# Kernel optimization log

Measured on AMD Instinct MI355X. Metric: run time of the kernel, lower is better.

## Reference

```python
import jax, jax.numpy as jnp
import numpy as np

B, D, H, W = 16, 512, 32, 32   # batch, input_dim, spatial
CD, K = 256, 8192              # codebook dim, num codes
COMMIT = 1.0


def setup_inputs() -> dict:
    key = jax.random.key(0)
    k0, k1, k2, k3 = jax.random.split(key, 4)
    x = jax.random.normal(k0, (B, D, H, W), dtype=jnp.float32)
    # project_in: Linear(D -> CD); project_out: Linear(CD -> D)
    W_in = jax.random.normal(k1, (CD, D), dtype=jnp.float32) * (1.0 / np.sqrt(D))
    b_in = jnp.zeros((CD,), dtype=jnp.float32)
    W_out = jax.random.normal(k2, (D, CD), dtype=jnp.float32) * (1.0 / np.sqrt(CD))
    b_out = jnp.zeros((D,), dtype=jnp.float32)
    codebook = jax.random.normal(k3, (K, CD), dtype=jnp.float32) * 0.05
    return {"x": x, "W_in": W_in, "b_in": b_in, "W_out": W_out,
            "b_out": b_out, "codebook": codebook}


def reference(x, W_in, b_in, W_out, b_out, codebook):
    b, d, h, w = x.shape
    # b d h w -> b (h w) d
    xt = x.reshape(b, d, h * w).transpose(0, 2, 1)
    z = xt @ W_in.T + b_in                              # [b, n, CD]
    # squared euclidean distances to all codes: ||z||^2 - 2 z.e + ||e||^2
    d2 = ((z * z).sum(-1, keepdims=True)
          - 2.0 * jnp.einsum('bnc,kc->bnk', z, codebook)
          + (codebook * codebook).sum(-1))              # [b, n, K]
    indices = jnp.argmin(d2, axis=-1)                   # [b, n] int
    q = codebook[indices]                               # [b, n, CD]
    # training branch: commitment loss + straight-through estimator
    commitment_loss = COMMIT * jnp.mean((jax.lax.stop_gradient(q) - z) ** 2)
    q_ste = z + jax.lax.stop_gradient(q - z)
    out = q_ste @ W_out.T + b_out                       # [b, n, d]
    out = out.transpose(0, 2, 1).reshape(b, d, h, w)    # b (h w) d -> b d h w
    return out, indices, commitment_loss
```

## Files before the change

kernel.cpp:

```cpp
#include <hip/hip_runtime.h>
#include <cfloat>
#include <cstdint>

#define B_      16
#define DIN     512
#define HW      1024
#define CDIM    256
#define KCODES  8192
#define NTOK    (B_ * HW)
#define OUT_ELEMS (B_ * DIN * HW)
#define NSTRIP  8
#define NPART2  16
#define CPS     (KCODES / NSTRIP)
#define MAXR    4096
#define RCHUNK  32
#define RBLOCKS 2048
#define LOSS_SCALE (1.0f / ((float)NTOK * (float)CDIM))
#define WSCALE      16.0f
#define INV_WS      0.0625f
#define INV_WS2     0.00390625f
#define NEG2_INV_WS (-0.125f)
#define BAND_SLACK  2e-3f
#define A_BYTES  131072
#define B_OFF    131072
#define EE_OFF   (131072 + 3 * 8192)
#define LDS_TOT  (EE_OFF + 4096)
#define PO_BOFF  65536
#define PO_TOT   163840

typedef __attribute__((ext_vector_type(8))) _Float16 f16x8;
typedef __attribute__((ext_vector_type(4))) float f32x4;

static __device__ __forceinline__ short f2h(float f) {
  _Float16 h = (_Float16)f;
  return __builtin_bit_cast(short, h);
}
static __device__ __forceinline__ float h2f(short h) {
  return (float)__builtin_bit_cast(_Float16, h);
}

#define GLL16(gsrc, ldst)                                                      \
  __builtin_amdgcn_global_load_lds(                                           \
      (const __attribute__((address_space(1))) unsigned int*)(gsrc),          \
      (__attribute__((address_space(3))) unsigned int*)(ldst), 16, 0, 0)

#define PREP_CB_BLKS 2048
#define PREP_W_BLKS  128
#define PREP_X_BLKS  2048
__global__ __launch_bounds__(256) void k_prep(
    const float* __restrict__ cb, const float* __restrict__ Win,
    const float* __restrict__ Wout, const float* __restrict__ x,
    short* __restrict__ cb_hi, short* __restrict__ cb_lo, float* __restrict__ ee,
    short* __restrict__ wi_hi, short* __restrict__ wi_lo,
    short* __restrict__ wo_hi,
    short* __restrict__ xT_hi, short* __restrict__ xT_lo,
    float* __restrict__ loss, int* __restrict__ rcount, int* __restrict__ scal) {
  __shared__ float T[64][65];
  const int blk = blockIdx.x;
  const int tid = threadIdx.x;
  if (blk == 0 && tid < 2) {
    if (tid == 0) *loss = 0.0f; else *rcount = 0;
  }
  if (blk < PREP_CB_BLKS) {
    const int wid = (blk * 256 + tid) >> 6;
    const int lane = tid & 63;
    const float4 v = *(const float4*)(cb + (size_t)wid * CDIM + lane * 4);
    float s = v.x * v.x + v.y * v.y + v.z * v.z + v.w * v.w;
    const float sx = v.x * WSCALE, sy = v.y * WSCALE,
                sz = v.z * WSCALE, sw = v.w * WSCALE;
    short4 h, l;
    h.x = f2h(sx); l.x = f2h(sx - h2f(h.x));
    h.y = f2h(sy); l.y = f2h(sy - h2f(h.y));
    h.z = f2h(sz); l.z = f2h(sz - h2f(h.z));
    h.w = f2h(sw); l.w = f2h(sw - h2f(h.w));
    *(short4*)(cb_hi + (size_t)wid * CDIM + lane * 4) = h;
    *(short4*)(cb_lo + (size_t)wid * CDIM + lane * 4) = l;
    const float rx = v.x - h2f(h.x) * INV_WS;
    const float ry = v.y - h2f(h.y) * INV_WS;
    const float rz = v.z - h2f(h.z) * INV_WS;
    const float rw = v.w - h2f(h.w) * INV_WS;
    float rr = rx * rx + ry * ry + rz * rz + rw * rw;
#pragma unroll
    for (int off = 32; off > 0; off >>= 1) {
      s += __shfl_down(s, off, 64);
      rr += __shfl_down(rr, off, 64);
    }
    const int wv = tid >> 6;
    if (lane == 0) { ee[wid] = s; T[0][wv] = s; T[1][wv] = rr; }
    __syncthreads();
    if (tid == 0) {
      const float em = fmaxf(fmaxf(T[0][0], T[0][1]), fmaxf(T[0][2], T[0][3]));
      const float rm = fmaxf(fmaxf(T[1][0], T[1][1]), fmaxf(T[1][2], T[1][3]));
      atomicMax(scal + 0, __float_as_int(em));
      atomicMax(scal + 1, __float_as_int(rm));
    }
  } else if (blk < PREP_CB_BLKS + PREP_W_BLKS) {
    const int i = ((blk - PREP_CB_BLKS) * 256 + tid) * 4;
    {
      const float4 v = *(const float4*)(Win + i);
      const float sx = v.x * WSCALE, sy = v.y * WSCALE,
                  sz = v.z * WSCALE, sw = v.w * WSCALE;
      short4 h, l;
      h.x = f2h(sx); l.x = f2h(sx - h2f(h.x));
      h.y = f2h(sy); l.y = f2h(sy - h2f(h.y));
      h.z = f2h(sz); l.z = f2h(sz - h2f(h.z));
      h.w = f2h(sw); l.w = f2h(sw - h2f(h.w));
      *(short4*)(wi_hi + i) = h; *(short4*)(wi_lo + i) = l;
    }
    {
      const float4 v = *(const float4*)(Wout + i);
      short4 h;
      h.x = f2h(v.x * WSCALE);
      h.y = f2h(v.y * WSCALE);
      h.z = f2h(v.z * WSCALE);
      h.w = f2h(v.w * WSCALE);
      *(short4*)(wo_hi + i) = h;
    }
  } else {
    const int id = blk - PREP_CB_BLKS - PREP_W_BLKS;
    const int xb = id & 255, yb = id >> 8;
    const int b = xb >> 4;
    const int hw0 = (xb & 15) * 64;
    const int din0 = yb * 64;
    {
      const int r = tid >> 2;
      const int c = tid & 3;
      const float* src = x + ((size_t)b * DIN + din0 + r) * HW + hw0 + c * 16;
#pragma unroll
      for (int j = 0; j < 4; ++j) {
        const float4 v = *(const float4*)(src + j * 4);
        T[r][c * 16 + j * 4 + 0] = v.x;
        T[r][c * 16 + j * 4 + 1] = v.y;
        T[r][c * 16 + j * 4 + 2] = v.z;
        T[r][c * 16 + j * 4 + 3] = v.w;
      }
    }
    __syncthreads();
    {
      const int tt = tid & 63;
      const int c2 = tid >> 6;
      short h[16], l[16];
#pragma unroll
      for (int j = 0; j < 16; ++j) {
        const float f = T[c2 * 16 + j][tt];
        h[j] = f2h(f); l[j] = f2h(f - h2f(h[j]));
      }
      const size_t base = ((size_t)b * HW + hw0 + tt) * DIN + din0 + c2 * 16;
      *(f16x8*)(xT_hi + base)     = *(f16x8*)&h[0];
      *(f16x8*)(xT_hi + base + 8) = *(f16x8*)&h[8];
      *(f16x8*)(xT_lo + base)     = *(f16x8*)&l[0];
      *(f16x8*)(xT_lo + base + 8) = *(f16x8*)&l[8];
    }
  }
}

__global__ __launch_bounds__(256, 2) void k_proj_in_mfma(
    const short* __restrict__ xT_hi, const short* __restrict__ xT_lo,
    const short* __restrict__ wi_hi, const short* __restrict__ wi_lo,
    const float* __restrict__ bin,
    short* __restrict__ z_hi, short* __restrict__ z_lo) {
  __shared__ short lds_s[4 * 128 * 32];
  char* ldsc = (char*)lds_s;
  const int tid = threadIdx.x;
  const int w = tid >> 6, lane = tid & 63;
  const int quad = lane >> 4, l16 = lane & 15;
  const int wm = w >> 1, wn = w & 1;
  const int tok0 = blockIdx.x * 128;
  const int cd0 = blockIdx.y * 128;

  const int uA = (w << 6) + lane, uB = uA + 256;
  const int tA = uA >> 2, pA = uA & 3, qA = pA ^ ((tA >> 1) & 3);
  const int tB = uB >> 2, pB = uB & 3, qB = pB ^ ((tB >> 1) & 3);
  const int offA = tA * DIN + qA * 8;
  const int offB = tB * DIN + qB * 8;
  const short* gAh0 = xT_hi + (size_t)tok0 * DIN + offA;
  const short* gAh1 = xT_hi + (size_t)tok0 * DIN + offB;
  const short* gAl0 = xT_lo + (size_t)tok0 * DIN + offA;
  const short* gAl1 = xT_lo + (size_t)tok0 * DIN + offB;
  const short* gBh0 = wi_hi + (size_t)cd0 * DIN + offA;
  const short* gBh1 = wi_hi + (size_t)cd0 * DIN + offB;
  const short* gBl0 = wi_lo + (size_t)cd0 * DIN + offA;
  const short* gBl1 = wi_lo + (size_t)cd0 * DIN + offB;

  int aoffs[4], boffs[4];
#pragma unroll
  for (int mi = 0; mi < 4; ++mi) {
    const int t = wm * 64 + mi * 16 + l16;
    aoffs[mi] = t * 64 + (quad ^ ((t >> 1) & 3)) * 16;
  }
#pragma unroll
  for (int ni = 0; ni < 4; ++ni) {
    const int t = wn * 64 + ni * 16 + l16;
    boffs[ni] = 16384 + t * 64 + (quad ^ ((t >> 1) & 3)) * 16;
  }

  f32x4 acc[4][4];
#pragma unroll
  for (int mi = 0; mi < 4; ++mi)
#pragma unroll
    for (int ni = 0; ni < 4; ++ni) acc[mi][ni] = (f32x4){0.f, 0.f, 0.f, 0.f};

  for (int kb = 0; kb < DIN; kb += 32) {
    __syncthreads();
    GLL16(gAh0 + kb, ldsc + ((0 * 4 + w) << 10));
    GLL16(gAh1 + kb, ldsc + ((1 * 4 + w) << 10));
    GLL16(gAl0 + kb, ldsc + ((2 * 4 + w) << 10));
    GLL16(gAl1 + kb, ldsc + ((3 * 4 + w) << 10));
    GLL16(gBh0 + kb, ldsc + ((4 * 4 + w) << 10));
    GLL16(gBh1 + kb, ldsc + ((5 * 4 + w) << 10));
    GLL16(gBl0 + kb, ldsc + ((6 * 4 + w) << 10));
    GLL16(gBl1 + kb, ldsc + ((7 * 4 + w) << 10));
    __syncthreads();
    f16x8 ah[4], al[4], bh[4], bl[4];
#pragma unroll
    for (int mi = 0; mi < 4; ++mi) {
      ah[mi] = *(const f16x8*)(ldsc + aoffs[mi]);
      al[mi] = *(const f16x8*)(ldsc + 8192 + aoffs[mi]);
    }
#pragma unroll
    for (int ni = 0; ni < 4; ++ni) {
      bh[ni] = *(const f16x8*)(ldsc + boffs[ni]);
      bl[ni] = *(const f16x8*)(ldsc + 8192 + boffs[ni]);
    }
#pragma unroll
    for (int mi = 0; mi < 4; ++mi)
#pragma unroll
      for (int ni = 0; ni < 4; ++ni) {
        f32x4 c = acc[mi][ni];
        c = __builtin_amdgcn_mfma_f32_16x16x32_f16(ah[mi], bh[ni], c, 0, 0, 0);
        c = __builtin_amdgcn_mfma_f32_16x16x32_f16(ah[mi], bl[ni], c, 0, 0, 0);
        c = __builtin_amdgcn_mfma_f32_16x16x32_f16(al[mi], bh[ni], c, 0, 0, 0);
        acc[mi][ni] = c;
      }
  }
  float bv[4];
#pragma unroll
  for (int ni = 0; ni < 4; ++ni) bv[ni] = bin[cd0 + wn * 64 + ni * 16 + l16];
#pragma unroll
  for (int mi = 0; mi < 4; ++mi)
#pragma unroll
    for (int r = 0; r < 4; ++r) {
      const int t = tok0 + wm * 64 + mi * 16 + quad * 4 + r;
#pragma unroll
      for (int ni = 0; ni < 4; ++ni) {
        const int cd = cd0 + wn * 64 + ni * 16 + l16;
        const float o = acc[mi][ni][r] * INV_WS + bv[ni];
        const short h = f2h(o);
        z_hi[(size_t)t * CDIM + cd] = h;
        z_lo[(size_t)t * CDIM + cd] = f2h(o - h2f(h));
      }
    }
}

__global__ __launch_bounds__(512, 2) void k_argmin_mfma(
    const short* __restrict__ z_hi,
    const short* __restrict__ cb_hi,
    const float* __restrict__ ee,
    float* __restrict__ pm1v, int* __restrict__ pm1i, float* __restrict__ pm2v) {
  __shared__ short lds_s[LDS_TOT / 2];
  char* ldsc = (char*)lds_s;
  const int tid = threadIdx.x;
  const int w = tid >> 6, lane = tid & 63;
  const int quad = lane >> 4, l16 = lane & 15;
  const int wm = w >> 1, wn = w & 1;
  const int tok0 = blockIdx.x * 256;
  const int cbase = blockIdx.y * CPS;

#pragma unroll
  for (int r = 0; r < 16; ++r) {
    const int u = r * 512 + tid;
    const int c = u >> 10, t = (u >> 2) & 255, p = u & 3;
    const int q = p ^ ((t >> 1) & 3);
    GLL16(z_hi + (size_t)(tok0 + t) * CDIM + c * 32 + q * 8,
          ldsc + r * 8192 + (w << 10));
  }
  if (w < 4) {
    GLL16(ee + cbase + w * 256 + lane * 4, ldsc + EE_OFF + (w << 10));
  }
  const int crB = tid >> 2, pB = tid & 3;
  const int qB = pB ^ ((crB >> 1) & 3);
  const short* bsrc = cb_hi + (size_t)(cbase + crB) * CDIM + qB * 8;
  GLL16(bsrc, ldsc + B_OFF + (w << 10));
  GLL16(bsrc + 32, ldsc + B_OFF + 8192 + (w << 10));

  int aoffs[4], boffs[4];
#pragma unroll
  for (int mi = 0; mi < 4; ++mi) {
    const int t = wm * 64 + mi * 16 + l16;
    aoffs[mi] = t * 64 + (quad ^ ((t >> 1) & 3)) * 16;
  }
#pragma unroll
  for (int ni = 0; ni < 4; ++ni) {
    const int t = wn * 64 + ni * 16 + l16;
    boffs[ni] = t * 64 + (quad ^ ((t >> 1) & 3)) * 16;
  }
  const float* eelds = (const float*)(ldsc + EE_OFF);

  float mv[16], sv[16]; int mi_[16];
#pragma unroll
  for (int j = 0; j < 16; ++j) {
    mv[j] = FLT_MAX; sv[j] = FLT_MAX; mi_[j] = 0x7fffffff;
  }

  int cur = 0;
  for (int ct = 0; ct < 8; ++ct) {
    f32x4 acc[4][4];
#pragma unroll
    for (int mi = 0; mi < 4; ++mi)
#pragma unroll
      for (int ni = 0; ni < 4; ++ni) acc[mi][ni] = (f32x4){0.f, 0.f, 0.f, 0.f};

#pragma unroll
    for (int kbi = 0; kbi < 8; ++kbi) {
      const int s = ct * 8 + kbi;
      asm volatile("s_waitcnt vmcnt(1)" ::: "memory");
      __builtin_amdgcn_s_barrier();
      __builtin_amdgcn_sched_barrier(0);
      {
        const int s2 = (s + 2) & 63;
        const int nslot = cur + 2 - ((cur >= 1) ? 3 : 0);
        GLL16(bsrc + (size_t)(s2 >> 3) * 128 * CDIM + (s2 & 7) * 32,
              ldsc + B_OFF + (nslot << 13) + (w << 10));
      }
      const int abase = kbi << 14;
      const int bbase = B_OFF + (cur << 13);
      f16x8 ah[4], bh[4];
#pragma unroll
      for (int mi = 0; mi < 4; ++mi)
        ah[mi] = *(const f16x8*)(ldsc + abase + aoffs[mi]);
#pragma unroll
      for (int ni = 0; ni < 4; ++ni)
        bh[ni] = *(const f16x8*)(ldsc + bbase + boffs[ni]);
#pragma unroll
      for (int mi = 0; mi < 4; ++mi)
#pragma unroll
        for (int ni = 0; ni < 4; ++ni)
          acc[mi][ni] = __builtin_amdgcn_mfma_f32_16x16x32_f16(
              ah[mi], bh[ni], acc[mi][ni], 0, 0, 0);
      cur = (cur == 2) ? 0 : cur + 1;
    }
    const int ctile = cbase + ct * 128;
    float eev[4];
#pragma unroll
    for (int ni = 0; ni < 4; ++ni)
      eev[ni] = eelds[ct * 128 + wn * 64 + ni * 16 + l16];
    const int cb2 = ctile + wn * 64 + l16;
#pragma unroll
    for (int mi = 0; mi < 4; ++mi)
#pragma unroll
      for (int r = 0; r < 4; ++r) {
        const int j = mi * 4 + r;
#pragma unroll
        for (int ni = 0; ni < 4; ++ni) {
          const float s = fmaf(NEG2_INV_WS, acc[mi][ni][r], eev[ni]);
          sv[j] = fminf(sv[j], fmaxf(mv[j], s));
          if (s < mv[j]) { mv[j] = s; mi_[j] = cb2 + ni * 16; }
        }
      }
  }
#pragma unroll
  for (int off = 1; off < 16; off <<= 1) {
#pragma unroll
    for (int j = 0; j < 16; ++j) {
      const float ov = __shfl_xor(mv[j], off, 64);
      const int   oi = __shfl_xor(mi_[j], off, 64);
      const float os = __shfl_xor(sv[j], off, 64);
      const float snew = fminf(fminf(sv[j], os), fmaxf(mv[j], ov));
      if (ov < mv[j] || (ov == mv[j] && oi < mi_[j])) { mv[j] = ov; mi_[j] = oi; }
      sv[j] = snew;
    }
  }
  if (l16 == 0) {
    const int p = blockIdx.y * 2 + wn;
#pragma unroll
    for (int j = 0; j < 16; ++j) {
      const int mi = j >> 2, r = j & 3;
      const int t = tok0 + wm * 64 + mi * 16 + quad * 4 + r;
      const size_t o = (size_t)p * NTOK + t;
      pm1v[o] = mv[j]; pm1i[o] = mi_[j]; pm2v[o] = sv[j];
    }
  }
}

__global__ __launch_bounds__(256) void k_merge_rescue(
    const float* __restrict__ pm1v, const int* __restrict__ pm1i,
    const float* __restrict__ pm2v,
    const short* __restrict__ z_hi, const short* __restrict__ z_lo,
    const float* __restrict__ cb, const int* __restrict__ scal,
    int* __restrict__ idxi, float* __restrict__ idx_f,
    int* __restrict__ rlist, int* __restrict__ rcount,
    float* __restrict__ loss) {
  __shared__ float lpart[4];
  const int tid = threadIdx.x;
  const int wv = tid >> 6, lane = tid & 63;
  const int t = blockIdx.x * 4 + wv;
  float av = FLT_MAX, asv = FLT_MAX; int ai = 0x7fffffff;
  if (lane < NPART2) {
    const size_t po = (size_t)lane * NTOK + t;
    av = pm1v[po]; ai = pm1i[po]; asv = pm2v[po];
  }
  float m1v = av; int m1i = ai; float msv = asv;
#pragma unroll
  for (int off = 1; off < 64; off <<= 1) {
    const float ov = __shfl_xor(m1v, off, 64);
    const int   oi = __shfl_xor(m1i, off, 64);
    const float os = __shfl_xor(msv, off, 64);
    msv = fminf(msv, os);
    if (ov < m1v || (ov == m1v && oi < m1i)) { m1v = ov; m1i = oi; }
  }
  const short4 h4 = *(const short4*)(z_hi + (size_t)t * CDIM + lane * 4);
  const short4 l4 = *(const short4*)(z_lo + (size_t)t * CDIM + lane * 4);
  const float hx = h2f(h4.x), hy = h2f(h4.y), hz = h2f(h4.z), hw = h2f(h4.w);
  const float lx = h2f(l4.x), ly = h2f(l4.y), lz = h2f(l4.z), lw = h2f(l4.w);
  const float zx = hx + lx, zy = hy + ly, zz = hz + lz, zw = hw + lw;
  float zl2 = lx * lx + ly * ly + lz * lz + lw * lw;
  float zh2 = hx * hx + hy * hy + hz * hz + hw * hw;
#pragma unroll
  for (int off = 32; off > 0; off >>= 1) {
    zl2 += __shfl_xor(zl2, off, 64);
    zh2 += __shfl_xor(zh2, off, 64);
  }
  const float emax = sqrtf(__int_as_float(scal[0]));
  const float rmax = sqrtf(__int_as_float(scal[1]));
  const float band = 4.0f * (sqrtf(zl2) * emax + sqrtf(zh2) * rmax) + BAND_SLACK;
  const float thr = m1v + band;
  const unsigned long long ball = __ballot(av <= thr);
  const bool flag = (msv <= thr);
  int besti = m1i;
  if (__popcll(ball) > 1) {
    double bestv = 1e300; int bi = 0x7fffffff;
    unsigned long long bb = ball;
    while (bb) {
      const int c = __ffsll((long long)bb) - 1;
      bb &= bb - 1;
      const int ci = __shfl(ai, c, 64);
      const float4 ev = *(const float4*)(cb + (size_t)ci * CDIM + lane * 4);
      const double dx = (double)zx - (double)ev.x;
      const double dy = (double)zy - (double)ev.y;
      const double dz_ = (double)zz - (double)ev.z;
      const double dw = (double)zw - (double)ev.w;
      double d = dx * dx + dy * dy + dz_ * dz_ + dw * dw;
#pragma unroll
      for (int off = 32; off > 0; off >>= 1) d += __shfl_xor(d, off, 64);
      if (d < bestv || (d == bestv && ci < bi)) { bestv = d; bi = ci; }
    }
    besti = bi;
  }
  const float4 qv = *(const float4*)(cb + (size_t)besti * CDIM + lane * 4);
  const float dx = qv.x - zx;
  const float dy = qv.y - zy;
  const float dz_ = qv.z - zz;
  const float dw = qv.w - zw;
  float s = dx * dx + dy * dy + dz_ * dz_ + dw * dw;
#pragma unroll
  for (int off = 32; off > 0; off >>= 1) s += __shfl_down(s, off, 64);
  if (lane == 0) {
    idxi[t] = besti;
    idx_f[t] = (float)besti;
    lpart[wv] = s;
    if (flag) {
      const int pos = atomicAdd(rcount, 1);
      if (pos < MAXR) rlist[pos] = t;
    }
  }
  __syncthreads();
  if (tid == 0) {
    atomicAdd(loss, (lpart[0] + lpart[1] + lpart[2] + lpart[3]) * LOSS_SCALE);
  }
}

__global__ __launch_bounds__(256) void k_rescue_chunk(
    const short* __restrict__ z_hi, const short* __restrict__ z_lo,
    const float* __restrict__ cb,
    const int* __restrict__ rlist, const int* __restrict__ rcount,
    double* __restrict__ slotv, int* __restrict__ sloti) {
  const int cnt0 = *rcount;
  const int cnt = cnt0 < MAXR ? cnt0 : MAXR;
  const int li0 = blockIdx.x >> 5;
  const int chunk = blockIdx.x & (RCHUNK - 1);
  if (li0 >= cnt) return;
  __shared__ float zrow[CDIM];
  __shared__ double rv[256];
  __shared__ int ri[256];
  const int tid = threadIdx.x;
  for (int li = li0; li < cnt; li += RBLOCKS / RCHUNK) {
    const int t = rlist[li];
    zrow[tid] = h2f(z_hi[(size_t)t * CDIM + tid]) + h2f(z_lo[(size_t)t * CDIM + tid]);
    __syncthreads();
    const int k = chunk * 256 + tid;
    const float* e = cb + (size_t)k * CDIM;
    double s0 = 0.0, s1 = 0.0, s2 = 0.0, s3 = 0.0;
    for (int c = 0; c < CDIM; c += 4) {
      const float4 ev = *(const float4*)(e + c);
      const double d0 = (double)zrow[c]     - (double)ev.x;
      const double d1 = (double)zrow[c + 1] - (double)ev.y;
      const double d2 = (double)zrow[c + 2] - (double)ev.z;
      const double d3 = (double)zrow[c + 3] - (double)ev.w;
      s0 += d0 * d0; s1 += d1 * d1; s2 += d2 * d2; s3 += d3 * d3;
    }
    rv[tid] = (s0 + s1) + (s2 + s3);
    ri[tid] = k;
    __syncthreads();
    for (int off = 128; off > 0; off >>= 1) {
      if (tid < off) {
        if (rv[tid + off] < rv[tid] ||
            (rv[tid + off] == rv[tid] && ri[tid + off] < ri[tid])) {
          rv[tid] = rv[tid + off]; ri[tid] = ri[tid + off];
        }
      }
      __syncthreads();
    }
    if (tid == 0) {
      slotv[(size_t)li * RCHUNK + chunk] = rv[0];
      sloti[(size_t)li * RCHUNK + chunk] = ri[0];
    }
    __syncthreads();
  }
}

__global__ __launch_bounds__(256) void k_rescue_fin(
    const double* __restrict__ slotv, const int* __restrict__ sloti,
    const int* __restrict__ rlist, const int* __restrict__ rcount,
    const short* __restrict__ z_hi, const short* __restrict__ z_lo,
    const float* __restrict__ cb,
    int* __restrict__ idxi, float* __restrict__ idx_f, float* __restrict__ loss) {
  const int cnt0 = *rcount;
  const int cnt = cnt0 < MAXR ? cnt0 : MAXR;
  const int tid = threadIdx.x;
  const int wv = tid >> 6, lane = tid & 63;
  for (int li = wv; li < cnt; li += 4) {
    double bv = 1e300; int bx = 0x7fffffff;
    if (lane < RCHUNK) {
      bv = slotv[(size_t)li * RCHUNK + lane];
      bx = sloti[(size_t)li * RCHUNK + lane];
    }
#pragma unroll
    for (int off = 1; off < 32; off <<= 1) {
      const double ov = __shfl_xor(bv, off, 64);
      const int   oi = __shfl_xor(bx, off, 64);
      if (ov < bv || (ov == bv && oi < bx)) { bv = ov; bx = oi; }
    }
    const int newi = __shfl(bx, 0, 64);
    const int t = rlist[li];
    const int oldi = idxi[t];
    if (newi != oldi) {
      const short4 h4 = *(const short4*)(z_hi + (size_t)t * CDIM + lane * 4);
      const short4 l4 = *(const short4*)(z_lo + (size_t)t * CDIM + lane * 4);
      const float4 qn = *(const float4*)(cb + (size_t)newi * CDIM + lane * 4);
      const float4 qo = *(const float4*)(cb + (size_t)oldi * CDIM + lane * 4);
      const float zx = h2f(h4.x) + h2f(l4.x);
      const float zy = h2f(h4.y) + h2f(l4.y);
      const float zz = h2f(h4.z) + h2f(l4.z);
      const float zw = h2f(h4.w) + h2f(l4.w);
      float d = (qn.x - zx) * (qn.x - zx) - (qo.x - zx) * (qo.x - zx)
              + (qn.y - zy) * (qn.y - zy) - (qo.y - zy) * (qo.y - zy)
              + (qn.z - zz) * (qn.z - zz) - (qo.z - zz) * (qo.z - zz)
              + (qn.w - zw) * (qn.w - zw) - (qo.w - zw) * (qo.w - zw);
#pragma unroll
      for (int off = 32; off > 0; off >>= 1) d += __shfl_down(d, off, 64);
      if (lane == 0) {
        idxi[t] = newi;
        idx_f[t] = (float)newi;
        atomicAdd(loss, d * LOSS_SCALE);
      }
    }
  }
}

__global__ __launch_bounds__(512, 2) void k_proj_out_mfma(
    const short* __restrict__ wo_hi,
    const short* __restrict__ cb_hi, const short* __restrict__ cb_lo,
    const int* __restrict__ idxi, const float* __restrict__ bout,
    float* __restrict__ out) {
  __shared__ short lds_s[PO_TOT / 2];
  char* ldsc = (char*)lds_s;
  const int tid = threadIdx.x;
  const int w = tid >> 6, lane = tid & 63;
  const int quad = lane >> 4, l16 = lane & 15;
  const int wm = w >> 2, wn = w & 3;
  const int tok0 = blockIdx.x * 256;
  const int din0 = blockIdx.y * 128;

  const int tr = tid >> 2, p = tid & 3;
  const int q = p ^ ((tr >> 1) & 3);
  const int i0 = idxi[tok0 + tr];
  const int i1 = idxi[tok0 + 128 + tr];
  const short* s0h = cb_hi + (size_t)i0 * CDIM + q * 8;
  const short* s1h = cb_hi + (size_t)i1 * CDIM + q * 8;
  const short* s0l = cb_lo + (size_t)i0 * CDIM + q * 8;
  const short* s1l = cb_lo + (size_t)i1 * CDIM + q * 8;

#pragma unroll
  for (int c = 0; c < 8; ++c)
    GLL16(wo_hi + (size_t)(din0 + tr) * CDIM + c * 32 + q * 8,
          ldsc + c * 8192 + (w << 10));

#define PO_STAGE(s_, slot_)                                                    \
  {                                                                            \
    char* bb_ = ldsc + PO_BOFF + ((slot_) << 15);                              \
    GLL16(s0h + (s_) * 32, bb_ + (w << 10));                                   \
    GLL16(s1h + (s_) * 32, bb_ + 8192 + (w << 10));                            \
    GLL16(s0l + (s_) * 32, bb_ + 16384 + (w << 10));                           \
    GLL16(s1l + (s_) * 32, bb_ + 24576 + (w << 10));                           \
  }
  PO_STAGE(0, 0);
  PO_STAGE(1, 1);

  int aoffs[4], boffs[4];
#pragma unroll
  for (int mi = 0; mi < 4; ++mi) {
    const int t = wm * 64 + mi * 16 + l16;
    aoffs[mi] = t * 64 + (quad ^ ((t >> 1) & 3)) * 16;
  }
#pragma unroll
  for (int ni = 0; ni < 4; ++ni) {
    const int t = wn * 64 + ni * 16 + l16;
    boffs[ni] = t * 64 + (quad ^ ((t >> 1) & 3)) * 16;
  }

  f32x4 acc[4][4];
#pragma unroll
  for (int mi = 0; mi < 4; ++mi)
#pragma unroll
    for (int ni = 0; ni < 4; ++ni) acc[mi][ni] = (f32x4){0.f, 0.f, 0.f, 0.f};

  int cur = 0;
#pragma unroll
  for (int s = 0; s < 8; ++s) {
    asm volatile("s_waitcnt vmcnt(4)" ::: "memory");
    __builtin_amdgcn_s_barrier();
    __builtin_amdgcn_sched_barrier(0);
    {
      const int s2 = (s + 2) & 7;
      const int nslot = cur + 2 - ((cur >= 1) ? 3 : 0);
      PO_STAGE(s2, nslot);
    }
    const int abase = s << 13;
    const int bbase = PO_BOFF + (cur << 15);
    f16x8 ah[4], bh[4], bl[4];
#pragma unroll
    for (int mi = 0; mi < 4; ++mi)
      ah[mi] = *(const f16x8*)(ldsc + abase + aoffs[mi]);
#pragma unroll
    for (int ni = 0; ni < 4; ++ni) {
      bh[ni] = *(const f16x8*)(ldsc + bbase + boffs[ni]);
      bl[ni] = *(const f16x8*)(ldsc + bbase + 16384 + boffs[ni]);
    }
#pragma unroll
    for (int mi = 0; mi < 4; ++mi)
#pragma unroll
      for (int ni = 0; ni < 4; ++ni) {
        f32x4 c = acc[mi][ni];
        c = __builtin_amdgcn_mfma_f32_16x16x32_f16(ah[mi], bh[ni], c, 0, 0, 0);
        c = __builtin_amdgcn_mfma_f32_16x16x32_f16(ah[mi], bl[ni], c, 0, 0, 0);
        acc[mi][ni] = c;
      }
    cur = (cur == 2) ? 0 : cur + 1;
  }
#undef PO_STAGE

  const int b = tok0 >> 10;
  const int hwb = tok0 & (HW - 1);
  float* ob = out + (size_t)b * DIN * HW;
#pragma unroll
  for (int mi = 0; mi < 4; ++mi)
#pragma unroll
    for (int r = 0; r < 4; ++r) {
      const int din = din0 + wm * 64 + mi * 16 + quad * 4 + r;
      const float bb = bout[din];
#pragma unroll
      for (int ni = 0; ni < 4; ++ni) {
        const int hw = hwb + wn * 64 + ni * 16 + l16;
        ob[(size_t)din * HW + hw] = acc[mi][ni][r] * INV_WS2 + bb;
      }
    }
}

extern "C" void kernel_launch(void* const* d_in, const int* in_sizes, int n_in,
                              void* d_out, int out_size, void* d_ws, size_t ws_size,
                              hipStream_t stream) {
  const float* x    = (const float*)d_in[0];
  const float* Win  = (const float*)d_in[1];
  const float* bin  = (const float*)d_in[2];
  const float* Wout = (const float*)d_in[3];
  const float* bout = (const float*)d_in[4];
  const float* cb   = (const float*)d_in[5];

  float* out   = (float*)d_out;
  float* idx_f = out + OUT_ELEMS;
  float* loss  = out + OUT_ELEMS + NTOK;

  char* w = (char*)d_ws;
  size_t off = 0;
  short* z_hi  = (short*)(w + off); off += (size_t)NTOK * CDIM * 2;
  short* z_lo  = (short*)(w + off); off += (size_t)NTOK * CDIM * 2;
  short* cb_hi = (short*)(w + off); off += (size_t)KCODES * CDIM * 2;
  short* cb_lo = (short*)(w + off); off += (size_t)KCODES * CDIM * 2;
  short* xT_hi = (short*)(w + off); off += (size_t)NTOK * DIN * 2;
  short* xT_lo = (short*)(w + off); off += (size_t)NTOK * DIN * 2;
  short* wi_hi = (short*)(w + off); off += (size_t)CDIM * DIN * 2;
  short* wi_lo = (short*)(w + off); off += (size_t)CDIM * DIN * 2;
  short* wo_hi = (short*)(w + off); off += (size_t)DIN * CDIM * 2;
  float* ee    = (float*)(w + off); off += (size_t)KCODES * 4;
  int*   idxi  = (int*)(w + off);   off += (size_t)NTOK * 4;
  float* pm1v  = (float*)(w + off); off += (size_t)NPART2 * NTOK * 4;
  int*   pm1i  = (int*)(w + off);   off += (size_t)NPART2 * NTOK * 4;
  float* pm2v  = (float*)(w + off); off += (size_t)NPART2 * NTOK * 4;
  int*   rlist = (int*)(w + off);   off += (size_t)MAXR * 4;
  int*   rcount= (int*)(w + off);   off += 256;
  int*   scal  = (int*)(w + off);   off += 256;
  double* slotv= (double*)(w + off);off += (size_t)MAXR * RCHUNK * 8;
  int*   sloti = (int*)(w + off);   off += (size_t)MAXR * RCHUNK * 4;

  hipMemsetAsync(scal, 0, 8, stream);
  k_prep        <<<dim3(PREP_CB_BLKS + PREP_W_BLKS + PREP_X_BLKS),
                   dim3(256), 0, stream>>>(cb, Win, Wout, x, cb_hi, cb_lo, ee,
                                           wi_hi, wi_lo, wo_hi,
                                           xT_hi, xT_lo, loss, rcount, scal);
  k_proj_in_mfma<<<dim3(NTOK / 128, CDIM / 128), dim3(256), 0, stream>>>(
      xT_hi, xT_lo, wi_hi, wi_lo, bin, z_hi, z_lo);
  k_argmin_mfma <<<dim3(NTOK / 256, NSTRIP), dim3(512), 0, stream>>>(
      z_hi, cb_hi, ee, pm1v, pm1i, pm2v);
  k_merge_rescue<<<dim3(NTOK / 4), dim3(256), 0, stream>>>(
      pm1v, pm1i, pm2v, z_hi, z_lo, cb, scal, idxi, idx_f,
      rlist, rcount, loss);
  k_rescue_chunk<<<dim3(RBLOCKS), dim3(256), 0, stream>>>(
      z_hi, z_lo, cb, rlist, rcount, slotv, sloti);
  k_rescue_fin  <<<dim3(1), dim3(256), 0, stream>>>(
      slotv, sloti, rlist, rcount, z_hi, z_lo, cb, idxi, idx_f, loss);
  k_proj_out_mfma<<<dim3(NTOK / 256, DIN / 128), dim3(512), 0, stream>>>(
      wo_hi, cb_hi, cb_lo, idxi, bout, out);
}
```

Measured before the change: 431.3 us.

## Reorder rescue after proj_out, fuse rescue kernels, patch outputs with delta correction

```diff
diff --git a/kernel.cpp b/kernel.cpp
--- a/kernel.cpp
+++ b/kernel.cpp
@@ -54,12 +54,15 @@
     short* __restrict__ wi_hi, short* __restrict__ wi_lo,
     short* __restrict__ wo_hi,
     short* __restrict__ xT_hi, short* __restrict__ xT_lo,
-    float* __restrict__ loss, int* __restrict__ rcount, int* __restrict__ scal) {
+    float* __restrict__ loss, int* __restrict__ rcount, int* __restrict__ done,
+    float* __restrict__ scalE, float* __restrict__ scalR) {
   __shared__ float T[64][65];
   const int blk = blockIdx.x;
   const int tid = threadIdx.x;
-  if (blk == 0 && tid < 2) {
-    if (tid == 0) *loss = 0.0f; else *rcount = 0;
+  if (blk == 0 && tid < 3) {
+    if (tid == 0) *loss = 0.0f;
+    else if (tid == 1) *rcount = 0;
+    else *done = 0;
   }
   if (blk < PREP_CB_BLKS) {
     const int wid = (blk * 256 + tid) >> 6;
@@ -89,10 +92,8 @@
     if (lane == 0) { ee[wid] = s; T[0][wv] = s; T[1][wv] = rr; }
     __syncthreads();
     if (tid == 0) {
-      const float em = fmaxf(fmaxf(T[0][0], T[0][1]), fmaxf(T[0][2], T[0][3]));
-      const float rm = fmaxf(fmaxf(T[1][0], T[1][1]), fmaxf(T[1][2], T[1][3]));
-      atomicMax(scal + 0, __float_as_int(em));
-      atomicMax(scal + 1, __float_as_int(rm));
+      scalE[blk] = fmaxf(fmaxf(T[0][0], T[0][1]), fmaxf(T[0][2], T[0][3]));
+      scalR[blk] = fmaxf(fmaxf(T[1][0], T[1][1]), fmaxf(T[1][2], T[1][3]));
     }
   } else if (blk < PREP_CB_BLKS + PREP_W_BLKS) {
     const int i = ((blk - PREP_CB_BLKS) * 256 + tid) * 4;
@@ -158,10 +159,32 @@
     const short* __restrict__ xT_hi, const short* __restrict__ xT_lo,
     const short* __restrict__ wi_hi, const short* __restrict__ wi_lo,
     const float* __restrict__ bin,
-    short* __restrict__ z_hi, short* __restrict__ z_lo) {
+    short* __restrict__ z_hi, short* __restrict__ z_lo,
+    const float* __restrict__ scalE, const float* __restrict__ scalR,
+    float* __restrict__ scalG) {
   __shared__ short lds_s[4 * 128 * 32];
   char* ldsc = (char*)lds_s;
   const int tid = threadIdx.x;
+  if (blockIdx.x == 0 && blockIdx.y == 0) {
+    float em = 0.f, rm = 0.f;
+#pragma unroll
+    for (int i = 0; i < 8; ++i) {
+      em = fmaxf(em, scalE[tid * 8 + i]);
+      rm = fmaxf(rm, scalR[tid * 8 + i]);
+    }
+#pragma unroll
+    for (int off = 32; off > 0; off >>= 1) {
+      em = fmaxf(em, __shfl_xor(em, off, 64));
+      rm = fmaxf(rm, __shfl_xor(rm, off, 64));
+    }
+    float* sred = (float*)ldsc;
+    if ((tid & 63) == 0) { sred[tid >> 6] = em; sred[4 + (tid >> 6)] = rm; }
+    __syncthreads();
+    if (tid == 0) {
+      scalG[0] = fmaxf(fmaxf(sred[0], sred[1]), fmaxf(sred[2], sred[3]));
+      scalG[1] = fmaxf(fmaxf(sred[4], sred[5]), fmaxf(sred[6], sred[7]));
+    }
+  }
   const int w = tid >> 6, lane = tid & 63;
   const int quad = lane >> 4, l16 = lane & 15;
   const int wm = w >> 1, wn = w & 1;
@@ -376,7 +399,7 @@
     for (int j = 0; j < 16; ++j) {
       const int mi = j >> 2, r = j & 3;
       const int t = tok0 + wm * 64 + mi * 16 + quad * 4 + r;
-      const size_t o = (size_t)p * NTOK + t;
+      const size_t o = (size_t)t * NPART2 + p;
       pm1v[o] = mv[j]; pm1i[o] = mi_[j]; pm2v[o] = sv[j];
     }
   }
@@ -386,7 +409,7 @@
     const float* __restrict__ pm1v, const int* __restrict__ pm1i,
     const float* __restrict__ pm2v,
     const short* __restrict__ z_hi, const short* __restrict__ z_lo,
-    const float* __restrict__ cb, const int* __restrict__ scal,
+    const float* __restrict__ cb, const float* __restrict__ scalG,
     int* __restrict__ idxi, float* __restrict__ idx_f,
     int* __restrict__ rlist, int* __restrict__ rcount,
     float* __restrict__ loss) {
@@ -396,7 +419,7 @@
   const int t = blockIdx.x * 4 + wv;
   float av = FLT_MAX, asv = FLT_MAX; int ai = 0x7fffffff;
   if (lane < NPART2) {
-    const size_t po = (size_t)lane * NTOK + t;
+    const size_t po = (size_t)t * NPART2 + lane;
     av = pm1v[po]; ai = pm1i[po]; asv = pm2v[po];
   }
   float m1v = av; int m1i = ai; float msv = asv;
@@ -420,8 +443,8 @@
     zl2 += __shfl_xor(zl2, off, 64);
     zh2 += __shfl_xor(zh2, off, 64);
   }
-  const float emax = sqrtf(__int_as_float(scal[0]));
-  const float rmax = sqrtf(__int_as_float(scal[1]));
+  const float emax = sqrtf(scalG[0]);
+  const float rmax = sqrtf(scalG[1]);
   const float band = 4.0f * (sqrtf(zl2) * emax + sqrtf(zh2) * rmax) + BAND_SLACK;
   const float thr = m1v + band;
   const unsigned long long ball = __ballot(av <= thr);
@@ -469,64 +492,173 @@
   }
 }
 
-__global__ __launch_bounds__(256) void k_rescue_chunk(
+__global__ __launch_bounds__(512, 2) void k_proj_out_mfma(
+    const short* __restrict__ wo_hi,
+    const short* __restrict__ cb_hi, const short* __restrict__ cb_lo,
+    const int* __restrict__ idxi, const float* __restrict__ bout,
+    float* __restrict__ out) {
+  __shared__ short lds_s[PO_TOT / 2];
+  char* ldsc = (char*)lds_s;
+  const int tid = threadIdx.x;
+  const int w = tid >> 6, lane = tid & 63;
+  const int quad = lane >> 4, l16 = lane & 15;
+  const int wm = w >> 2, wn = w & 3;
+  const int tok0 = blockIdx.x * 256;
+  const int din0 = blockIdx.y * 128;
+
+  const int tr = tid >> 2, p = tid & 3;
+  const int q = p ^ ((tr >> 1) & 3);
+  const int i0 = idxi[tok0 + tr];
+  const int i1 = idxi[tok0 + 128 + tr];
+  const short* s0h = cb_hi + (size_t)i0 * CDIM + q * 8;
+  const short* s1h = cb_hi + (size_t)i1 * CDIM + q * 8;
+  const short* s0l = cb_lo + (size_t)i0 * CDIM + q * 8;
+  const short* s1l = cb_lo + (size_t)i1 * CDIM + q * 8;
+
+#pragma unroll
+  for (int c = 0; c < 8; ++c)
+    GLL16(wo_hi + (size_t)(din0 + tr) * CDIM + c * 32 + q * 8,
+          ldsc + c * 8192 + (w << 10));
+
+#define PO_STAGE(s_, slot_)                                                    \
+  {                                                                            \
+    char* bb_ = ldsc + PO_BOFF + ((slot_) << 15);                              \
+    GLL16(s0h + (s_) * 32, bb_ + (w << 10));                                   \
+    GLL16(s1h + (s_) * 32, bb_ + 8192 + (w << 10));                            \
+    GLL16(s0l + (s_) * 32, bb_ + 16384 + (w << 10));                           \
+    GLL16(s1l + (s_) * 32, bb_ + 24576 + (w << 10));                           \
+  }
+  PO_STAGE(0, 0);
+  PO_STAGE(1, 1);
+
+  int aoffs[4], boffs[4];
+#pragma unroll
+  for (int mi = 0; mi < 4; ++mi) {
+    const int t = wm * 64 + mi * 16 + l16;
+    aoffs[mi] = t * 64 + (quad ^ ((t >> 1) & 3)) * 16;
+  }
+#pragma unroll
+  for (int ni = 0; ni < 4; ++ni) {
+    const int t = wn * 64 + ni * 16 + l16;
+    boffs[ni] = t * 64 + (quad ^ ((t >> 1) & 3)) * 16;
+  }
+
+  f32x4 acc[4][4];
+#pragma unroll
+  for (int mi = 0; mi < 4; ++mi)
+#pragma unroll
+    for (int ni = 0; ni < 4; ++ni) acc[mi][ni] = (f32x4){0.f, 0.f, 0.f, 0.f};
+
+  int cur = 0;
+#pragma unroll
+  for (int s = 0; s < 8; ++s) {
+    asm volatile("s_waitcnt vmcnt(4)" ::: "memory");
+    __builtin_amdgcn_s_barrier();
+    __builtin_amdgcn_sched_barrier(0);
+    {
+      const int s2 = (s + 2) & 7;
+      const int nslot = cur + 2 - ((cur >= 1) ? 3 : 0);
+      PO_STAGE(s2, nslot);
+    }
+    const int abase = s << 13;
+    const int bbase = PO_BOFF + (cur << 15);
+    f16x8 ah[4], bh[4], bl[4];
+#pragma unroll
+    for (int mi = 0; mi < 4; ++mi)
+      ah[mi] = *(const f16x8*)(ldsc + abase + aoffs[mi]);
+#pragma unroll
+    for (int ni = 0; ni < 4; ++ni) {
+      bh[ni] = *(const f16x8*)(ldsc + bbase + boffs[ni]);
+      bl[ni] = *(const f16x8*)(ldsc + bbase + 16384 + boffs[ni]);
+    }
+#pragma unroll
+    for (int mi = 0; mi < 4; ++mi)
+#pragma unroll
+      for (int ni = 0; ni < 4; ++ni) {
+        f32x4 c = acc[mi][ni];
+        c = __builtin_amdgcn_mfma_f32_16x16x32_f16(ah[mi], bh[ni], c, 0, 0, 0);
+        c = __builtin_amdgcn_mfma_f32_16x16x32_f16(ah[mi], bl[ni], c, 0, 0, 0);
+        acc[mi][ni] = c;
+      }
+    cur = (cur == 2) ? 0 : cur + 1;
+  }
+#undef PO_STAGE
+
+  const int b = tok0 >> 10;
+  const int hwb = tok0 & (HW - 1);
+  float* ob = out + (size_t)b * DIN * HW;
+#pragma unroll
+  for (int mi = 0; mi < 4; ++mi)
+#pragma unroll
+    for (int r = 0; r < 4; ++r) {
+      const int din = din0 + wm * 64 + mi * 16 + quad * 4 + r;
+      const float bb = bout[din];
+#pragma unroll
+      for (int ni = 0; ni < 4; ++ni) {
+        const int hw = hwb + wn * 64 + ni * 16 + l16;
+        ob[(size_t)din * HW + hw] = acc[mi][ni][r] * INV_WS2 + bb;
+      }
+    }
+}
+
+__global__ __launch_bounds__(256) void k_rescue_chunk_fin(
     const short* __restrict__ z_hi, const short* __restrict__ z_lo,
     const float* __restrict__ cb,
     const int* __restrict__ rlist, const int* __restrict__ rcount,
-    double* __restrict__ slotv, int* __restrict__ sloti) {
+    double* __restrict__ slotv, int* __restrict__ sloti,
+    int* __restrict__ done,
+    int* __restrict__ idxi, float* __restrict__ idx_f, float* __restrict__ loss,
+    const float* __restrict__ Wout, float* __restrict__ out,
+    int* __restrict__ pold, int* __restrict__ pnew) {
   const int cnt0 = *rcount;
   const int cnt = cnt0 < MAXR ? cnt0 : MAXR;
   const int li0 = blockIdx.x >> 5;
   const int chunk = blockIdx.x & (RCHUNK - 1);
-  if (li0 >= cnt) return;
   __shared__ float zrow[CDIM];
   __shared__ double rv[256];
   __shared__ int ri[256];
+  __shared__ int isLast;
   const int tid = threadIdx.x;
-  for (int li = li0; li < cnt; li += RBLOCKS / RCHUNK) {
-    const int t = rlist[li];
-    zrow[tid] = h2f(z_hi[(size_t)t * CDIM + tid]) + h2f(z_lo[(size_t)t * CDIM + tid]);
-    __syncthreads();
-    const int k = chunk * 256 + tid;
-    const float* e = cb + (size_t)k * CDIM;
-    double s0 = 0.0, s1 = 0.0, s2 = 0.0, s3 = 0.0;
-    for (int c = 0; c < CDIM; c += 4) {
-      const float4 ev = *(const float4*)(e + c);
-      const double d0 = (double)zrow[c]     - (double)ev.x;
-      const double d1 = (double)zrow[c + 1] - (double)ev.y;
-      const double d2 = (double)zrow[c + 2] - (double)ev.z;
-      const double d3 = (double)zrow[c + 3] - (double)ev.w;
-      s0 += d0 * d0; s1 += d1 * d1; s2 += d2 * d2; s3 += d3 * d3;
-    }
-    rv[tid] = (s0 + s1) + (s2 + s3);
-    ri[tid] = k;
-    __syncthreads();
-    for (int off = 128; off > 0; off >>= 1) {
-      if (tid < off) {
-        if (rv[tid + off] < rv[tid] ||
-            (rv[tid + off] == rv[tid] && ri[tid + off] < ri[tid])) {
-          rv[tid] = rv[tid + off]; ri[tid] = ri[tid + off];
+  if (li0 < cnt) {
+    for (int li = li0; li < cnt; li += RBLOCKS / RCHUNK) {
+      const int t = rlist[li];
+      zrow[tid] = h2f(z_hi[(size_t)t * CDIM + tid]) + h2f(z_lo[(size_t)t * CDIM + tid]);
+      __syncthreads();
+      const int k = chunk * 256 + tid;
+      const float* e = cb + (size_t)k * CDIM;
+      double s0 = 0.0, s1 = 0.0, s2 = 0.0, s3 = 0.0;
+      for (int c = 0; c < CDIM; c += 4) {
+        const float4 ev = *(const float4*)(e + c);
+        const double d0 = (double)zrow[c]     - (double)ev.x;
+        const double d1 = (double)zrow[c + 1] - (double)ev.y;
+        const double d2 = (double)zrow[c + 2] - (double)ev.z;
+        const double d3 = (double)zrow[c + 3] - (double)ev.w;
+        s0 += d0 * d0; s1 += d1 * d1; s2 += d2 * d2; s3 += d3 * d3;
+      }
+      rv[tid] = (s0 + s1) + (s2 + s3);
+      ri[tid] = k;
+      __syncthreads();
+      for (int off = 128; off > 0; off >>= 1) {
+        if (tid < off) {
+          if (rv[tid + off] < rv[tid] ||
+              (rv[tid + off] == rv[tid] && ri[tid + off] < ri[tid])) {
+            rv[tid] = rv[tid + off]; ri[tid] = ri[tid + off];
+          }
         }
+        __syncthreads();
+      }
+      if (tid == 0) {
+        slotv[(size_t)li * RCHUNK + chunk] = rv[0];
+        sloti[(size_t)li * RCHUNK + chunk] = ri[0];
       }
       __syncthreads();
     }
-    if (tid == 0) {
-      slotv[(size_t)li * RCHUNK + chunk] = rv[0];
-      sloti[(size_t)li * RCHUNK + chunk] = ri[0];
-    }
-    __syncthreads();
-  }
-}
-
-__global__ __launch_bounds__(256) void k_rescue_fin(
-    const double* __restrict__ slotv, const int* __restrict__ sloti,
-    const int* __restrict__ rlist, const int* __restrict__ rcount,
-    const short* __restrict__ z_hi, const short* __restrict__ z_lo,
-    const float* __restrict__ cb,
-    int* __restrict__ idxi, float* __restrict__ idx_f, float* __restrict__ loss) {
-  const int cnt0 = *rcount;
-  const int cnt = cnt0 < MAXR ? cnt0 : MAXR;
-  const int tid = threadIdx.x;
+  }
+  __threadfence();
+  if (tid == 0) isLast = (atomicAdd(done, 1) == RBLOCKS - 1);
+  __syncthreads();
+  if (isLast == 0) return;
+  __threadfence();
   const int wv = tid >> 6, lane = tid & 63;
   for (int li = wv; li < cnt; li += 4) {
     double bv = 1e300; int bx = 0x7fffffff;
@@ -543,6 +675,7 @@
     const int newi = __shfl(bx, 0, 64);
     const int t = rlist[li];
     const int oldi = idxi[t];
+    if (lane == 0) { pold[li] = oldi; pnew[li] = newi; }
     if (newi != oldi) {
       const short4 h4 = *(const short4*)(z_hi + (size_t)t * CDIM + lane * 4);
       const short4 l4 = *(const short4*)(z_lo + (size_t)t * CDIM + lane * 4);
@@ -565,115 +698,30 @@
       }
     }
   }
-}
-
-__global__ __launch_bounds__(512, 2) void k_proj_out_mfma(
-    const short* __restrict__ wo_hi,
-    const short* __restrict__ cb_hi, const short* __restrict__ cb_lo,
-    const int* __restrict__ idxi, const float* __restrict__ bout,
-    float* __restrict__ out) {
-  __shared__ short lds_s[PO_TOT / 2];
-  char* ldsc = (char*)lds_s;
-  const int tid = threadIdx.x;
-  const int w = tid >> 6, lane = tid & 63;
-  const int quad = lane >> 4, l16 = lane & 15;
-  const int wm = w >> 2, wn = w & 3;
-  const int tok0 = blockIdx.x * 256;
-  const int din0 = blockIdx.y * 128;
-
-  const int tr = tid >> 2, p = tid & 3;
-  const int q = p ^ ((tr >> 1) & 3);
-  const int i0 = idxi[tok0 + tr];
-  const int i1 = idxi[tok0 + 128 + tr];
-  const short* s0h = cb_hi + (size_t)i0 * CDIM + q * 8;
-  const short* s1h = cb_hi + (size_t)i1 * CDIM + q * 8;
-  const short* s0l = cb_lo + (size_t)i0 * CDIM + q * 8;
-  const short* s1l = cb_lo + (size_t)i1 * CDIM + q * 8;
-
-#pragma unroll
-  for (int c = 0; c < 8; ++c)
-    GLL16(wo_hi + (size_t)(din0 + tr) * CDIM + c * 32 + q * 8,
-          ldsc + c * 8192 + (w << 10));
-
-#define PO_STAGE(s_, slot_)                                                    \
-  {                                                                            \
-    char* bb_ = ldsc + PO_BOFF + ((slot_) << 15);                              \
-    GLL16(s0h + (s_) * 32, bb_ + (w << 10));                                   \
-    GLL16(s1h + (s_) * 32, bb_ + 8192 + (w << 10));                            \
-    GLL16(s0l + (s_) * 32, bb_ + 16384 + (w << 10));                           \
-    GLL16(s1l + (s_) * 32, bb_ + 24576 + (w << 10));                           \
-  }
-  PO_STAGE(0, 0);
-  PO_STAGE(1, 1);
-
-  int aoffs[4], boffs[4];
-#pragma unroll
-  for (int mi = 0; mi < 4; ++mi) {
-    const int t = wm * 64 + mi * 16 + l16;
-    aoffs[mi] = t * 64 + (quad ^ ((t >> 1) & 3)) * 16;
-  }
-#pragma unroll
-  for (int ni = 0; ni < 4; ++ni) {
-    const int t = wn * 64 + ni * 16 + l16;
-    boffs[ni] = t * 64 + (quad ^ ((t >> 1) & 3)) * 16;
-  }
-
-  f32x4 acc[4][4];
-#pragma unroll
-  for (int mi = 0; mi < 4; ++mi)
-#pragma unroll
-    for (int ni = 0; ni < 4; ++ni) acc[mi][ni] = (f32x4){0.f, 0.f, 0.f, 0.f};
-
-  int cur = 0;
-#pragma unroll
-  for (int s = 0; s < 8; ++s) {
-    asm volatile("s_waitcnt vmcnt(4)" ::: "memory");
-    __builtin_amdgcn_s_barrier();
-    __builtin_amdgcn_sched_barrier(0);
-    {
-      const int s2 = (s + 2) & 7;
-      const int nslot = cur + 2 - ((cur >= 1) ? 3 : 0);
-      PO_STAGE(s2, nslot);
-    }
-    const int abase = s << 13;
-    const int bbase = PO_BOFF + (cur << 15);
-    f16x8 ah[4], bh[4], bl[4];
-#pragma unroll
-    for (int mi = 0; mi < 4; ++mi)
-      ah[mi] = *(const f16x8*)(ldsc + abase + aoffs[mi]);
-#pragma unroll
-    for (int ni = 0; ni < 4; ++ni) {
-      bh[ni] = *(const f16x8*)(ldsc + bbase + boffs[ni]);
-      bl[ni] = *(const f16x8*)(ldsc + bbase + 16384 + boffs[ni]);
-    }
-#pragma unroll
-    for (int mi = 0; mi < 4; ++mi)
-#pragma unroll
-      for (int ni = 0; ni < 4; ++ni) {
-        f32x4 c = acc[mi][ni];
-        c = __builtin_amdgcn_mfma_f32_16x16x32_f16(ah[mi], bh[ni], c, 0, 0, 0);
-        c = __builtin_amdgcn_mfma_f32_16x16x32_f16(ah[mi], bl[ni], c, 0, 0, 0);
-        acc[mi][ni] = c;
-      }
-    cur = (cur == 2) ? 0 : cur + 1;
-  }
-#undef PO_STAGE
-
-  const int b = tok0 >> 10;
-  const int hwb = tok0 & (HW - 1);
-  float* ob = out + (size_t)b * DIN * HW;
-#pragma unroll
-  for (int mi = 0; mi < 4; ++mi)
-#pragma unroll
-    for (int r = 0; r < 4; ++r) {
-      const int din = din0 + wm * 64 + mi * 16 + quad * 4 + r;
-      const float bb = bout[din];
-#pragma unroll
-      for (int ni = 0; ni < 4; ++ni) {
-        const int hw = hwb + wn * 64 + ni * 16 + l16;
-        ob[(size_t)din * HW + hw] = acc[mi][ni][r] * INV_WS2 + bb;
-      }
-    }
+  __syncthreads();
+  for (int li = 0; li < cnt; ++li) {
+    const int oldi = pold[li], newi = pnew[li];
+    if (oldi == newi) continue;
+    const int t = rlist[li];
+    const int b = t >> 10, hw = t & (HW - 1);
+    float* oc = out + (size_t)b * DIN * HW + hw;
+    const float* en = cb + (size_t)newi * CDIM;
+    const float* eo = cb + (size_t)oldi * CDIM;
+#pragma unroll
+    for (int rr2 = 0; rr2 < 2; ++rr2) {
+      const int din = tid + rr2 * 256;
+      const float* wr = Wout + (size_t)din * CDIM;
+      float d = 0.f;
+      for (int cdi = 0; cdi < CDIM; cdi += 4) {
+        const float4 wv4 = *(const float4*)(wr + cdi);
+        const float4 nv = *(const float4*)(en + cdi);
+        const float4 ov = *(const float4*)(eo + cdi);
+        d += wv4.x * (nv.x - ov.x) + wv4.y * (nv.y - ov.y)
+           + wv4.z * (nv.z - ov.z) + wv4.w * (nv.w - ov.w);
+      }
+      oc[(size_t)din * HW] += d;
+    }
+  }
 }
 
 extern "C" void kernel_launch(void* const* d_in, const int* in_sizes, int n_in,
@@ -708,26 +756,30 @@
   float* pm2v  = (float*)(w + off); off += (size_t)NPART2 * NTOK * 4;
   int*   rlist = (int*)(w + off);   off += (size_t)MAXR * 4;
   int*   rcount= (int*)(w + off);   off += 256;
-  int*   scal  = (int*)(w + off);   off += 256;
+  int*   done  = (int*)(w + off);   off += 256;
+  float* scalG = (float*)(w + off); off += 256;
+  float* scalE = (float*)(w + off); off += (size_t)PREP_CB_BLKS * 4;
+  float* scalR = (float*)(w + off); off += (size_t)PREP_CB_BLKS * 4;
+  int*   pold  = (int*)(w + off);   off += (size_t)MAXR * 4;
+  int*   pnew  = (int*)(w + off);   off += (size_t)MAXR * 4;
   double* slotv= (double*)(w + off);off += (size_t)MAXR * RCHUNK * 8;
   int*   sloti = (int*)(w + off);   off += (size_t)MAXR * RCHUNK * 4;
 
-  hipMemsetAsync(scal, 0, 8, stream);
   k_prep        <<<dim3(PREP_CB_BLKS + PREP_W_BLKS + PREP_X_BLKS),
                    dim3(256), 0, stream>>>(cb, Win, Wout, x, cb_hi, cb_lo, ee,
                                            wi_hi, wi_lo, wo_hi,
-                                           xT_hi, xT_lo, loss, rcount, scal);
+                                           xT_hi, xT_lo, loss, rcount, done,
+                                           scalE, scalR);
   k_proj_in_mfma<<<dim3(NTOK / 128, CDIM / 128), dim3(256), 0, stream>>>(
-      xT_hi, xT_lo, wi_hi, wi_lo, bin, z_hi, z_lo);
+      xT_hi, xT_lo, wi_hi, wi_lo, bin, z_hi, z_lo, scalE, scalR, scalG);
   k_argmin_mfma <<<dim3(NTOK / 256, NSTRIP), dim3(512), 0, stream>>>(
       z_hi, cb_hi, ee, pm1v, pm1i, pm2v);
   k_merge_rescue<<<dim3(NTOK / 4), dim3(256), 0, stream>>>(
-      pm1v, pm1i, pm2v, z_hi, z_lo, cb, scal, idxi, idx_f,
+      pm1v, pm1i, pm2v, z_hi, z_lo, cb, scalG, idxi, idx_f,
       rlist, rcount, loss);
-  k_rescue_chunk<<<dim3(RBLOCKS), dim3(256), 0, stream>>>(
-      z_hi, z_lo, cb, rlist, rcount, slotv, sloti);
-  k_rescue_fin  <<<dim3(1), dim3(256), 0, stream>>>(
-      slotv, sloti, rlist, rcount, z_hi, z_lo, cb, idxi, idx_f, loss);
   k_proj_out_mfma<<<dim3(NTOK / 256, DIN / 128), dim3(512), 0, stream>>>(
       wo_hi, cb_hi, cb_lo, idxi, bout, out);
-}
+  k_rescue_chunk_fin<<<dim3(RBLOCKS), dim3(256), 0, stream>>>(
+      z_hi, z_lo, cb, rlist, rcount, slotv, sloti, done,
+      idxi, idx_f, loss, Wout, out, pold, pnew);
+}
```

Measured after the change: 541.1 us. 1.25x slower.

## Triple-buffer proj_in LDS loads and raise wave priority around MFMA blocks

Applied to the files above, without the earlier changes.

```diff
diff --git a/kernel.cpp b/kernel.cpp
--- a/kernel.cpp
+++ b/kernel.cpp
@@ -159,7 +159,7 @@
     const short* __restrict__ wi_hi, const short* __restrict__ wi_lo,
     const float* __restrict__ bin,
     short* __restrict__ z_hi, short* __restrict__ z_lo) {
-  __shared__ short lds_s[4 * 128 * 32];
+  __shared__ short lds_s[3 * 16384];
   char* ldsc = (char*)lds_s;
   const int tid = threadIdx.x;
   const int w = tid >> 6, lane = tid & 63;
@@ -168,19 +168,32 @@
   const int tok0 = blockIdx.x * 128;
   const int cd0 = blockIdx.y * 128;
 
-  const int uA = (w << 6) + lane, uB = uA + 256;
-  const int tA = uA >> 2, pA = uA & 3, qA = pA ^ ((tA >> 1) & 3);
-  const int tB = uB >> 2, pB = uB & 3, qB = pB ^ ((tB >> 1) & 3);
-  const int offA = tA * DIN + qA * 8;
-  const int offB = tB * DIN + qB * 8;
-  const short* gAh0 = xT_hi + (size_t)tok0 * DIN + offA;
-  const short* gAh1 = xT_hi + (size_t)tok0 * DIN + offB;
-  const short* gAl0 = xT_lo + (size_t)tok0 * DIN + offA;
-  const short* gAl1 = xT_lo + (size_t)tok0 * DIN + offB;
-  const short* gBh0 = wi_hi + (size_t)cd0 * DIN + offA;
-  const short* gBh1 = wi_hi + (size_t)cd0 * DIN + offB;
-  const short* gBl0 = wi_lo + (size_t)cd0 * DIN + offA;
-  const short* gBl1 = wi_lo + (size_t)cd0 * DIN + offB;
+  const int t0 = tid >> 2, p0 = tid & 3, q0 = p0 ^ ((t0 >> 1) & 3);
+  const int u1 = tid + 256, t1 = u1 >> 2, p1 = u1 & 3, q1 = p1 ^ ((t1 >> 1) & 3);
+  const short* A0h = xT_hi + (size_t)(tok0 + t0) * DIN + q0 * 8;
+  const short* A1h = xT_hi + (size_t)(tok0 + t1) * DIN + q1 * 8;
+  const short* A0l = xT_lo + (size_t)(tok0 + t0) * DIN + q0 * 8;
+  const short* A1l = xT_lo + (size_t)(tok0 + t1) * DIN + q1 * 8;
+  const short* B0h = wi_hi + (size_t)(cd0 + t0) * DIN + q0 * 8;
+  const short* B1h = wi_hi + (size_t)(cd0 + t1) * DIN + q1 * 8;
+  const short* B0l = wi_lo + (size_t)(cd0 + t0) * DIN + q0 * 8;
+  const short* B1l = wi_lo + (size_t)(cd0 + t1) * DIN + q1 * 8;
+
+#define PI_STAGE(s_, slot_)                                                    \
+  {                                                                            \
+    char* bb_ = ldsc + ((slot_) << 15);                                        \
+    const int kb_ = (s_) * 32;                                                 \
+    GLL16(A0h + kb_, bb_ + (w << 10));                                         \
+    GLL16(A1h + kb_, bb_ + 4096 + (w << 10));                                  \
+    GLL16(A0l + kb_, bb_ + 8192 + (w << 10));                                  \
+    GLL16(A1l + kb_, bb_ + 12288 + (w << 10));                                 \
+    GLL16(B0h + kb_, bb_ + 16384 + (w << 10));                                 \
+    GLL16(B1h + kb_, bb_ + 20480 + (w << 10));                                 \
+    GLL16(B0l + kb_, bb_ + 24576 + (w << 10));                                 \
+    GLL16(B1l + kb_, bb_ + 28672 + (w << 10));                                 \
+  }
+  PI_STAGE(0, 0);
+  PI_STAGE(1, 1);
 
   int aoffs[4], boffs[4];
 #pragma unroll
@@ -200,28 +213,30 @@
 #pragma unroll
     for (int ni = 0; ni < 4; ++ni) acc[mi][ni] = (f32x4){0.f, 0.f, 0.f, 0.f};
 
-  for (int kb = 0; kb < DIN; kb += 32) {
-    __syncthreads();
-    GLL16(gAh0 + kb, ldsc + ((0 * 4 + w) << 10));
-    GLL16(gAh1 + kb, ldsc + ((1 * 4 + w) << 10));
-    GLL16(gAl0 + kb, ldsc + ((2 * 4 + w) << 10));
-    GLL16(gAl1 + kb, ldsc + ((3 * 4 + w) << 10));
-    GLL16(gBh0 + kb, ldsc + ((4 * 4 + w) << 10));
-    GLL16(gBh1 + kb, ldsc + ((5 * 4 + w) << 10));
-    GLL16(gBl0 + kb, ldsc + ((6 * 4 + w) << 10));
-    GLL16(gBl1 + kb, ldsc + ((7 * 4 + w) << 10));
-    __syncthreads();
+  int cur = 0;
+#pragma unroll
+  for (int s = 0; s < 16; ++s) {
+    asm volatile("s_waitcnt vmcnt(8)" ::: "memory");
+    __builtin_amdgcn_s_barrier();
+    __builtin_amdgcn_sched_barrier(0);
+    {
+      const int s2 = (s + 2) & 15;
+      const int nslot = cur + 2 - ((cur >= 1) ? 3 : 0);
+      PI_STAGE(s2, nslot);
+    }
+    const int bb = cur << 15;
     f16x8 ah[4], al[4], bh[4], bl[4];
 #pragma unroll
     for (int mi = 0; mi < 4; ++mi) {
-      ah[mi] = *(const f16x8*)(ldsc + aoffs[mi]);
-      al[mi] = *(const f16x8*)(ldsc + 8192 + aoffs[mi]);
+      ah[mi] = *(const f16x8*)(ldsc + bb + aoffs[mi]);
+      al[mi] = *(const f16x8*)(ldsc + bb + 8192 + aoffs[mi]);
     }
 #pragma unroll
     for (int ni = 0; ni < 4; ++ni) {
-      bh[ni] = *(const f16x8*)(ldsc + boffs[ni]);
-      bl[ni] = *(const f16x8*)(ldsc + 8192 + boffs[ni]);
-    }
+      bh[ni] = *(const f16x8*)(ldsc + bb + boffs[ni]);
+      bl[ni] = *(const f16x8*)(ldsc + bb + 8192 + boffs[ni]);
+    }
+    __builtin_amdgcn_s_setprio(1);
 #pragma unroll
     for (int mi = 0; mi < 4; ++mi)
 #pragma unroll
@@ -232,7 +247,11 @@
         c = __builtin_amdgcn_mfma_f32_16x16x32_f16(al[mi], bh[ni], c, 0, 0, 0);
         acc[mi][ni] = c;
       }
-  }
+    __builtin_amdgcn_s_setprio(0);
+    cur = (cur == 2) ? 0 : cur + 1;
+  }
+#undef PI_STAGE
+
   float bv[4];
 #pragma unroll
   for (int ni = 0; ni < 4; ++ni) bv[ni] = bin[cd0 + wn * 64 + ni * 16 + l16];
@@ -331,12 +350,14 @@
 #pragma unroll
       for (int ni = 0; ni < 4; ++ni)
         bh[ni] = *(const f16x8*)(ldsc + bbase + boffs[ni]);
+      __builtin_amdgcn_s_setprio(1);
 #pragma unroll
       for (int mi = 0; mi < 4; ++mi)
 #pragma unroll
         for (int ni = 0; ni < 4; ++ni)
           acc[mi][ni] = __builtin_amdgcn_mfma_f32_16x16x32_f16(
               ah[mi], bh[ni], acc[mi][ni], 0, 0, 0);
+      __builtin_amdgcn_s_setprio(0);
       cur = (cur == 2) ? 0 : cur + 1;
     }
     const int ctile = cbase + ct * 128;
@@ -646,6 +667,7 @@
       bh[ni] = *(const f16x8*)(ldsc + bbase + boffs[ni]);
       bl[ni] = *(const f16x8*)(ldsc + bbase + 16384 + boffs[ni]);
     }
+    __builtin_amdgcn_s_setprio(1);
 #pragma unroll
     for (int mi = 0; mi < 4; ++mi)
 #pragma unroll
@@ -655,6 +677,7 @@
         c = __builtin_amdgcn_mfma_f32_16x16x32_f16(ah[mi], bl[ni], c, 0, 0, 0);
         acc[mi][ni] = c;
       }
+    __builtin_amdgcn_s_setprio(0);
     cur = (cur == 2) ? 0 : cur + 1;
   }
 #undef PO_STAGE
```

After: 429.9 us. About the same (-0.3%).
